# Kernel optimization log

Measured on AMD Instinct MI355X. Metric: run time of the kernel, lower is better.

Reference implementation:

```python
import jax, jax.numpy as jnp
import numpy as np

NUM_NODES = 100000
INPUT_DIM = 256
NUM_BAGS = 2048
BAG_SIZE = 64
N_EDGES = 3200000  # num_nodes * avg_degree(32)


def setup_inputs() -> dict:
    key = jax.random.key(0)
    ks = jax.random.split(key, 7)
    x = jax.random.normal(ks[0], (NUM_NODES, INPUT_DIM), dtype=jnp.float32)
    bags = jax.random.randint(ks[1], (NUM_BAGS, BAG_SIZE), 0, NUM_NODES)
    alpha_values = jax.random.uniform(ks[2], (NUM_BAGS, BAG_SIZE, 1), dtype=jnp.float32)
    # edge_dict in COO form: edge_src[e] has neighbor edge_nbr[e]
    edge_src = jax.random.randint(ks[3], (N_EDGES,), 0, NUM_NODES)
    edge_nbr = jax.random.randint(ks[4], (N_EDGES,), 0, NUM_NODES)
    node_weights = jax.random.uniform(ks[5], (NUM_NODES,), dtype=jnp.float32)  # torch.rand init
    theta_w = jax.random.normal(ks[6], (INPUT_DIM,), dtype=jnp.float32) / np.sqrt(INPUT_DIM)
    return dict(x=x, bags=bags, alpha_values=alpha_values, edge_src=edge_src,
                edge_nbr=edge_nbr, node_weights=node_weights, theta_w=theta_w)


def reference(x, bags, alpha_values, edge_src, edge_nbr, node_weights, theta_w):
    # Per-source neighbor weight sum: sum_value(source) = sum(node_weights[edge_dict[source]])
    nbr_sum = jax.ops.segment_sum(node_weights[edge_nbr], edge_src, num_segments=NUM_NODES)
    deg = jax.ops.segment_sum(jnp.ones_like(edge_src, dtype=x.dtype), edge_src,
                              num_segments=NUM_NODES)
    # sources not in edge_dict get sum_value = 1.0
    nbr_sum = jnp.where(deg > 0, nbr_sum, jnp.asarray(1.0, x.dtype))
    # h_values = theta(x[bag]); theta is Linear(input_dim, 1, bias=False)
    h = jnp.einsum('nbd,d->nb', x[bags], theta_w)          # [num_bags, bag_size]
    feat = h * alpha_values[..., 0]                         # [num_bags, bag_size]
    ns = nbr_sum[bags]                                      # [num_bags, bag_size]
    return jnp.sum(ns * feat, axis=1)                       # [num_bags]
```

## Files before the change

kernel.cpp:

```cpp
#include <hip/hip_runtime.h>

#define NUM_NODES 100000
#define INPUT_DIM 256
#define NUM_BAGS  2048
#define BAG_SIZE  64
#define N_EDGES   3200000
#define P_PART    8
#define NPP       12500
#define NSLICE    32
#define NQUAD     (N_EDGES / 4)

typedef unsigned int u32;

__global__ void __launch_bounds__(256)
mat_w(const int* __restrict__ edge_nbr, const float* __restrict__ nw,
      float* __restrict__ w) {
    const int q = blockIdx.x * 256 + threadIdx.x;
    const int4 n4 = ((const int4*)edge_nbr)[q];
    float4 o;
    o.x = nw[n4.x];
    o.y = nw[n4.y];
    o.z = nw[n4.z];
    o.w = nw[n4.w];
    ((float4*)w)[q] = o;
}

__global__ void __launch_bounds__(1024)
hist_kernel(const int* __restrict__ edge_src, const float* __restrict__ w,
            float* __restrict__ rep) {
    __shared__ float hist[NPP];
    const int i    = blockIdx.x;
    const int r    = i & 7;
    const int p    = (i >> 3) & 7;
    const int b    = r | ((i >> 6) << 3);
    const int base = p * NPP;

    for (int j = threadIdx.x; j < NPP; j += 1024) hist[j] = 0.f;
    __syncthreads();

    const int per = NQUAD / NSLICE;
    const int lo  = b * per;
    const int hi  = lo + per;
    for (int q = lo + (int)threadIdx.x; q < hi; q += 1024) {
        const int4   s4 = ((const int4*)edge_src)[q];
        const float4 w4 = ((const float4*)w)[q];
#define EDGE(S, W)                                               \
        {                                                        \
            const u32 rel = (u32)((S) - base);                   \
            if (rel < (u32)NPP) atomicAdd(&hist[rel], (W));      \
        }
        EDGE(s4.x, w4.x)
        EDGE(s4.y, w4.y)
        EDGE(s4.z, w4.z)
        EDGE(s4.w, w4.w)
#undef EDGE
    }
    __syncthreads();

    float* dst = rep + (size_t)b * NUM_NODES + base;
    for (int j = threadIdx.x; j < NPP; j += 1024)
        __builtin_nontemporal_store(hist[j], &dst[j]);
}

__global__ void __launch_bounds__(256)
reduce_rep(const float* __restrict__ rep, float* __restrict__ nbr_sum) {
    const int i = blockIdx.x * 256 + threadIdx.x;
    if (i >= NUM_NODES / 4) return;
    float4 a = make_float4(0.f, 0.f, 0.f, 0.f);
    for (int r = 0; r < NSLICE; ++r) {
        const float4 v = ((const float4*)(rep + (size_t)r * NUM_NODES))[i];
        a.x += v.x; a.y += v.y; a.z += v.z; a.w += v.w;
    }
    float4 o;
    o.x = a.x > 0.f ? a.x : 1.0f;
    o.y = a.y > 0.f ? a.y : 1.0f;
    o.z = a.z > 0.f ? a.z : 1.0f;
    o.w = a.w > 0.f ? a.w : 1.0f;
    ((float4*)nbr_sum)[i] = o;
}

__global__ void __launch_bounds__(256)
gemv_h(const float* __restrict__ x, const float* __restrict__ theta,
       float* __restrict__ h) {
    const int lane = threadIdx.x & 63;
    const int wave = threadIdx.x >> 6;
    const float4 tw = *reinterpret_cast<const float4*>(&theta[lane * 4]);
    const int stride = gridDim.x * 4;
    for (int row = blockIdx.x * 4 + wave; row < NUM_NODES; row += stride) {
        const float4 xv =
            *reinterpret_cast<const float4*>(&x[(size_t)row * INPUT_DIM + lane * 4]);
        float d = xv.x * tw.x + xv.y * tw.y + xv.z * tw.z + xv.w * tw.w;
        #pragma unroll
        for (int off = 32; off >= 1; off >>= 1)
            d += __shfl_xor(d, off);
        if (lane == 0) h[row] = d;
    }
}

__global__ void __launch_bounds__(256)
bag_final(const int* __restrict__ bags, const float* __restrict__ alpha,
          const float* __restrict__ h, const float* __restrict__ ns,
          float* __restrict__ out) {
    const int bag  = blockIdx.x * 4 + (threadIdx.x >> 6);
    const int lane = threadIdx.x & 63;
    const int idx  = bags[bag * BAG_SIZE + lane];
    float v = h[idx] * ns[idx] * alpha[bag * BAG_SIZE + lane];
    #pragma unroll
    for (int off = 32; off >= 1; off >>= 1)
        v += __shfl_xor(v, off);
    if (lane == 0) out[bag] = v;
}

__global__ void __launch_bounds__(256)
edge_atomic(const int* __restrict__ edge_src, const int* __restrict__ edge_nbr,
            const float* __restrict__ nw, float* __restrict__ nbr_sum) {
    const int t = blockIdx.x * blockDim.x + threadIdx.x;
    const int4 s4 = ((const int4*)edge_src)[t];
    const int4 n4 = ((const int4*)edge_nbr)[t];
    atomicAdd(&nbr_sum[s4.x], nw[n4.x]);
    atomicAdd(&nbr_sum[s4.y], nw[n4.y]);
    atomicAdd(&nbr_sum[s4.z], nw[n4.z]);
    atomicAdd(&nbr_sum[s4.w], nw[n4.w]);
}

__global__ void __launch_bounds__(256)
fixup_nosum(float* __restrict__ nbr_sum) {
    const int i = blockIdx.x * 256 + threadIdx.x;
    if (i < NUM_NODES && nbr_sum[i] == 0.f) nbr_sum[i] = 1.0f;
}

extern "C" void kernel_launch(void* const* d_in, const int* in_sizes, int n_in,
                              void* d_out, int out_size, void* d_ws, size_t ws_size,
                              hipStream_t stream) {
    const float* x            = (const float*)d_in[0];
    const int*   bags         = (const int*)d_in[1];
    const float* alpha        = (const float*)d_in[2];
    const int*   edge_src     = (const int*)d_in[3];
    const int*   edge_nbr     = (const int*)d_in[4];
    const float* node_weights = (const float*)d_in[5];
    const float* theta        = (const float*)d_in[6];
    float*       out          = (float*)d_out;

    const size_t need_full =
        ((size_t)N_EDGES + (size_t)NSLICE * NUM_NODES + 2 * (size_t)NUM_NODES) * 4;

    if (ws_size >= need_full) {
        float* w       = (float*)d_ws;
        float* rep     = w + N_EDGES;
        float* nbr_sum = rep + (size_t)NSLICE * NUM_NODES;
        float* h       = nbr_sum + NUM_NODES;

        mat_w<<<NQUAD / 256, 256, 0, stream>>>(edge_nbr, node_weights, w);
        hist_kernel<<<P_PART * NSLICE, 1024, 0, stream>>>(edge_src, w, rep);
        reduce_rep<<<(NUM_NODES / 4 + 255) / 256, 256, 0, stream>>>(rep, nbr_sum);
        gemv_h<<<2048, 256, 0, stream>>>(x, theta, h);
        bag_final<<<NUM_BAGS / 4, 256, 0, stream>>>(bags, alpha, h, nbr_sum, out);
    } else {
        float* nbr_sum = (float*)d_ws;
        float* h       = nbr_sum + NUM_NODES;
        hipMemsetAsync(nbr_sum, 0, (size_t)NUM_NODES * 4, stream);
        edge_atomic<<<(N_EDGES / 4) / 256, 256, 0, stream>>>(
            edge_src, edge_nbr, node_weights, nbr_sum);
        fixup_nosum<<<(NUM_NODES + 255) / 256, 256, 0, stream>>>(nbr_sum);
        gemv_h<<<2048, 256, 0, stream>>>(x, theta, h);
        bag_final<<<NUM_BAGS / 4, 256, 0, stream>>>(bags, alpha, h, nbr_sum, out);
    }
}
```

Measured before the change: 67.63 us.

## Assign histogram work units dynamically per XCD via atomic ticket counters

The histogram kernel now reads the hardware XCD id and takes a work unit from a per-XCD atomic ticket counter, stealing from other XCDs' queues once its own is empty. Each XCD's queue holds the four edge slices across all eight node partitions, so blocks that read the same edge slice land on the same XCD and can share its L2. The cost is an extra memset launch and a global atomic per block, and it relies on an undocumented hardware register layout for the XCD id.

```diff
diff --git a/kernel.cpp b/kernel.cpp
--- a/kernel.cpp
+++ b/kernel.cpp
@@ -5,12 +5,19 @@
 #define NUM_BAGS  2048
 #define BAG_SIZE  64
 #define N_EDGES   3200000
+#define NQUAD     (N_EDGES / 4)
 #define P_PART    8
 #define NPP       12500
 #define NSLICE    32
-#define NQUAD     (N_EDGES / 4)
+#define NXCD      8
+#define SLICES_PER_Q  (NSLICE / NXCD)
+#define UNITS_PER_Q   (SLICES_PER_Q * P_PART)
 
 typedef unsigned int u32;
+
+__device__ __forceinline__ u32 xcd_id() {
+    return __builtin_amdgcn_s_getreg(20 | (3 << 11)) & (NXCD - 1);
+}
 
 __global__ void __launch_bounds__(256)
 mat_w(const int* __restrict__ edge_nbr, const float* __restrict__ nw,
@@ -26,24 +33,40 @@
 }
 
 __global__ void __launch_bounds__(1024)
-hist_kernel(const int* __restrict__ edge_src, const float* __restrict__ w,
-            float* __restrict__ rep) {
+hist_t(const int* __restrict__ edge_src, const float* __restrict__ w,
+       float* __restrict__ rep,
+       u32* __restrict__ tick) {
     __shared__ float hist[NPP];
-    const int i    = blockIdx.x;
-    const int r    = i & 7;
-    const int p    = (i >> 3) & 7;
-    const int b    = r | ((i >> 6) << 3);
-    const int base = p * NPP;
+    __shared__ int s_unit;
 
+    if (threadIdx.x == 0) {
+        const u32 r = xcd_id();
+        int unit = -1;
+        #pragma unroll
+        for (int j = 0; j < NXCD; ++j) {
+            const u32 q = (r + j) & (NXCD - 1);
+            const u32 t = atomicAdd(&tick[q], 1u);
+            if (t < UNITS_PER_Q) { unit = (int)(q * UNITS_PER_Q + t); break; }
+        }
+        s_unit = unit;
+    }
     for (int j = threadIdx.x; j < NPP; j += 1024) hist[j] = 0.f;
     __syncthreads();
 
+    const int unit = s_unit;
+    if (unit < 0) return;
+    const int q     = unit / UNITS_PER_Q;
+    const int t     = unit % UNITS_PER_Q;
+    const int slice = q * SLICES_PER_Q + (t >> 3);
+    const int part  = t & 7;
+    const int base  = part * NPP;
+
     const int per = NQUAD / NSLICE;
-    const int lo  = b * per;
+    const int lo  = slice * per;
     const int hi  = lo + per;
-    for (int q = lo + (int)threadIdx.x; q < hi; q += 1024) {
-        const int4   s4 = ((const int4*)edge_src)[q];
-        const float4 w4 = ((const float4*)w)[q];
+    for (int i = lo + (int)threadIdx.x; i < hi; i += 1024) {
+        const int4   s4 = ((const int4*)edge_src)[i];
+        const float4 w4 = ((const float4*)w)[i];
 #define EDGE(S, W)                                               \
         {                                                        \
             const u32 rel = (u32)((S) - base);                   \
@@ -57,7 +80,7 @@
     }
     __syncthreads();
 
-    float* dst = rep + (size_t)b * NUM_NODES + base;
+    float* dst = rep + (size_t)slice * NUM_NODES + base;
     for (int j = threadIdx.x; j < NPP; j += 1024)
         __builtin_nontemporal_store(hist[j], &dst[j]);
 }
@@ -142,16 +165,19 @@
     float*       out          = (float*)d_out;
 
     const size_t need_full =
-        ((size_t)N_EDGES + (size_t)NSLICE * NUM_NODES + 2 * (size_t)NUM_NODES) * 4;
+        ((size_t)N_EDGES + (size_t)NSLICE * NUM_NODES + 2 * (size_t)NUM_NODES) * 4
+        + NXCD * sizeof(u32);
 
     if (ws_size >= need_full) {
         float* w       = (float*)d_ws;
         float* rep     = w + N_EDGES;
         float* nbr_sum = rep + (size_t)NSLICE * NUM_NODES;
         float* h       = nbr_sum + NUM_NODES;
+        u32*   tick    = (u32*)(h + NUM_NODES);
 
+        hipMemsetAsync(tick, 0, NXCD * sizeof(u32), stream);
         mat_w<<<NQUAD / 256, 256, 0, stream>>>(edge_nbr, node_weights, w);
-        hist_kernel<<<P_PART * NSLICE, 1024, 0, stream>>>(edge_src, w, rep);
+        hist_t<<<NSLICE * P_PART, 1024, 0, stream>>>(edge_src, w, rep, tick);
         reduce_rep<<<(NUM_NODES / 4 + 255) / 256, 256, 0, stream>>>(rep, nbr_sum);
         gemv_h<<<2048, 256, 0, stream>>>(x, theta, h);
         bag_final<<<NUM_BAGS / 4, 256, 0, stream>>>(bags, alpha, h, nbr_sum, out);
```

Measured after the change: 75.28 us. +11.3%, slower.

## Pack source index and bf16-rounded weight into one word per edge

Applied to the files above, without the earlier changes.

The preprocessing kernel now packs each edge's 17-bit source index and a 15-bit bf16-rounded node weight (sign bit dropped, weights assumed non-negative) into a single 32-bit word. The histogram kernel therefore reads 4 bytes per edge instead of 8 on each of its 8 partition passes. The number of edge slices doubles to 64, giving more histogram blocks, and small unroll pragmas are added. The trade-offs are a loss of weight precision, a replica buffer twice as large for the reduction to read, and a larger workspace requirement that could push execution onto the slower fallback path.

```diff
diff --git a/kernel.cpp b/kernel.cpp
--- a/kernel.cpp
+++ b/kernel.cpp
@@ -5,29 +5,32 @@
 #define NUM_BAGS  2048
 #define BAG_SIZE  64
 #define N_EDGES   3200000
+#define NQUAD     (N_EDGES / 4)
 #define P_PART    8
 #define NPP       12500
-#define NSLICE    32
-#define NQUAD     (N_EDGES / 4)
+#define NSLICE    64
 
 typedef unsigned int u32;
 
 __global__ void __launch_bounds__(256)
-mat_w(const int* __restrict__ edge_nbr, const float* __restrict__ nw,
-      float* __restrict__ w) {
+pack_edges(const int* __restrict__ edge_src, const int* __restrict__ edge_nbr,
+           const float* __restrict__ nw, u32* __restrict__ packed) {
     const int q = blockIdx.x * 256 + threadIdx.x;
+    const int4 s4 = ((const int4*)edge_src)[q];
     const int4 n4 = ((const int4*)edge_nbr)[q];
-    float4 o;
-    o.x = nw[n4.x];
-    o.y = nw[n4.y];
-    o.z = nw[n4.z];
-    o.w = nw[n4.w];
-    ((float4*)w)[q] = o;
+#define PACK(S, N)  (((u32)(S) << 15) |                                     \
+                     (((__float_as_uint(nw[(N)]) + 0x8000u) >> 16) & 0x7FFFu))
+    uint4 o;
+    o.x = PACK(s4.x, n4.x);
+    o.y = PACK(s4.y, n4.y);
+    o.z = PACK(s4.z, n4.z);
+    o.w = PACK(s4.w, n4.w);
+#undef PACK
+    ((uint4*)packed)[q] = o;
 }
 
 __global__ void __launch_bounds__(1024)
-hist_kernel(const int* __restrict__ edge_src, const float* __restrict__ w,
-            float* __restrict__ rep) {
+hist_p(const u32* __restrict__ packed, float* __restrict__ rep) {
     __shared__ float hist[NPP];
     const int i    = blockIdx.x;
     const int r    = i & 7;
@@ -41,18 +44,20 @@
     const int per = NQUAD / NSLICE;
     const int lo  = b * per;
     const int hi  = lo + per;
+    #pragma unroll 2
     for (int q = lo + (int)threadIdx.x; q < hi; q += 1024) {
-        const int4   s4 = ((const int4*)edge_src)[q];
-        const float4 w4 = ((const float4*)w)[q];
-#define EDGE(S, W)                                               \
-        {                                                        \
-            const u32 rel = (u32)((S) - base);                   \
-            if (rel < (u32)NPP) atomicAdd(&hist[rel], (W));      \
+        const uint4 w4 = ((const uint4*)packed)[q];
+#define EDGE(W)                                                          \
+        {                                                                \
+            const u32 rel = ((W) >> 15) - (u32)base;                     \
+            if (rel < (u32)NPP)                                          \
+                atomicAdd(&hist[rel],                                    \
+                          __uint_as_float(((W) & 0x7FFFu) << 16));       \
         }
-        EDGE(s4.x, w4.x)
-        EDGE(s4.y, w4.y)
-        EDGE(s4.z, w4.z)
-        EDGE(s4.w, w4.w)
+        EDGE(w4.x)
+        EDGE(w4.y)
+        EDGE(w4.z)
+        EDGE(w4.w)
 #undef EDGE
     }
     __syncthreads();
@@ -67,6 +72,7 @@
     const int i = blockIdx.x * 256 + threadIdx.x;
     if (i >= NUM_NODES / 4) return;
     float4 a = make_float4(0.f, 0.f, 0.f, 0.f);
+    #pragma unroll 8
     for (int r = 0; r < NSLICE; ++r) {
         const float4 v = ((const float4*)(rep + (size_t)r * NUM_NODES))[i];
         a.x += v.x; a.y += v.y; a.z += v.z; a.w += v.w;
@@ -145,13 +151,14 @@
         ((size_t)N_EDGES + (size_t)NSLICE * NUM_NODES + 2 * (size_t)NUM_NODES) * 4;
 
     if (ws_size >= need_full) {
-        float* w       = (float*)d_ws;
-        float* rep     = w + N_EDGES;
+        u32*   packed  = (u32*)d_ws;
+        float* rep     = (float*)d_ws + N_EDGES;
         float* nbr_sum = rep + (size_t)NSLICE * NUM_NODES;
         float* h       = nbr_sum + NUM_NODES;
 
-        mat_w<<<NQUAD / 256, 256, 0, stream>>>(edge_nbr, node_weights, w);
-        hist_kernel<<<P_PART * NSLICE, 1024, 0, stream>>>(edge_src, w, rep);
+        pack_edges<<<NQUAD / 256, 256, 0, stream>>>(edge_src, edge_nbr,
+                                                    node_weights, packed);
+        hist_p<<<P_PART * NSLICE, 1024, 0, stream>>>(packed, rep);
         reduce_rep<<<(NUM_NODES / 4 + 255) / 256, 256, 0, stream>>>(rep, nbr_sum);
         gemv_h<<<2048, 256, 0, stream>>>(x, theta, h);
         bag_final<<<NUM_BAGS / 4, 256, 0, stream>>>(bags, alpha, h, nbr_sum, out);
```

Result: slower. 72.01 us (+6.5%).
